# Performance work log

Measured on AMD Instinct MI355X. Metric: run time of the kernel, lower is better.

## Reference

```python
import jax, jax.numpy as jnp
import numpy as np

C = 2            # var_cardinality
ALPHA2 = 0.5     # global alpha2 skip coefficient referenced by the original module
A_FTOV = 0.5     # alpha_damping_FtoV
A_VTOF = 0.5     # alpha_damping_VtoF
SHIFT = 1e-19    # shifted ReLU offset (avoids log(0) in exp-space MLP)

V = 1_000_000    # num variables
F = 2_000_000    # num factors (pairwise)
E = 2 * F        # num factor->var edges


def setup_inputs() -> dict:
    key = jax.random.key(0)
    ks = jax.random.split(key, 6)
    # pairwise factors: factor f owns edges 2f (its dim-0 var) and 2f+1 (its dim-1 var)
    fac_idx = jnp.repeat(jnp.arange(F, dtype=jnp.int32), 2)          # [E]
    var_idx = jax.random.randint(ks[0], (E,), 0, V, dtype=jnp.int32)  # [E]
    edge_var_dim = jnp.tile(jnp.array([0, 1], dtype=jnp.int32), F)    # [E]
    eye = jnp.eye(C, dtype=jnp.float32)
    zc = jnp.zeros((C,), dtype=jnp.float32)
    return dict(
        prv_varToFactor_messages=jax.random.normal(ks[1], (E, C), dtype=jnp.float32),
        prv_factorToVar_messages=jax.random.normal(ks[2], (E, C), dtype=jnp.float32),
        prv_factor_beliefs=jax.random.normal(ks[3], (F, C, C), dtype=jnp.float32),
        factor_potentials=jax.random.normal(ks[4], (F, C, C), dtype=jnp.float32),
        W5=eye, b5=zc, W6=eye, b6=zc,          # mlp3 (factor->var), exact-BP init
        W7=eye, b7=zc, W8=eye, b8=zc,          # mlp4 (var->factor), exact-BP init
        alpha_mlp3=jnp.float32(ALPHA2), alpha_mlp4=jnp.float32(ALPHA2),
        fac_idx=fac_idx, var_idx=var_idx, edge_var_dim=edge_var_dim,
    )


def _mlp_exp_space(logm, W1, b1, W2, b2):
    # lne_mlp=True: exponentiate, run linear-relu-linear-shifted_relu, back to log space
    m = jnp.exp(logm)
    h = jax.nn.relu(m @ W1.T + b1)
    o = jax.nn.relu(h @ W2.T + b2) + SHIFT
    return jnp.log(o)


def _expand(msg, dim):
    # [E,C] per-edge message over its variable -> [E,C,C] over the factor's joint state,
    # broadcast along the factor dimension the edge does NOT own
    e0 = jnp.broadcast_to(msg[:, :, None], (msg.shape[0], C, C))
    e1 = jnp.broadcast_to(msg[:, None, :], (msg.shape[0], C, C))
    return jnp.where((dim == 0)[:, None, None], e0, e1)


def reference(prv_varToFactor_messages, prv_factorToVar_messages,
              prv_factor_beliefs, factor_potentials,
              W5, b5, W6, b6, W7, b7, W8, b8,
              alpha_mlp3, alpha_mlp4,
              fac_idx, var_idx, edge_var_dim):
    lse = jax.scipy.special.logsumexp
    # ---- factor -> variable messages (no double counting) ----
    mapped_fb = prv_factor_beliefs[fac_idx]                                  # gather [E,C,C]
    tmp = mapped_fb - _expand(prv_varToFactor_messages, edge_var_dim)        # subtract prv msg in log space
    marg = jnp.where((edge_var_dim == 0)[:, None],
                     lse(tmp, axis=2), lse(tmp, axis=1))                     # marginalize other var [E,C]
    ftv = alpha_mlp3 * marg + (1.0 - alpha_mlp3) * _mlp_exp_space(marg, W5, b5, W6, b6)
    ftv = A_FTOV * ftv + (1.0 - A_FTOV) * prv_factorToVar_messages           # damping
    ftv = ftv - lse(ftv, axis=1, keepdims=True)                              # normalize
    # ---- variable beliefs: log-space sum of incoming messages ----
    var_beliefs = jax.ops.segment_sum(ftv, var_idx, num_segments=V)          # [V,C]
    # ---- variable -> factor messages (no double counting) ----
    mapped_vb = var_beliefs[var_idx]                                         # gather [E,C]
    vtf_exact = mapped_vb - ftv
    vtf = alpha_mlp4 * vtf_exact + (1.0 - alpha_mlp4) * _mlp_exp_space(vtf_exact, W7, b7, W8, b8)
    vtf = A_VTOF * vtf + (1.0 - A_VTOF) * prv_varToFactor_messages           # damping
    vtf = vtf - lse(vtf, axis=1, keepdims=True)                              # normalize
    # ---- factor beliefs: scatter expanded messages + factor potentials ----
    expanded = _expand(vtf, edge_var_dim)                                    # [E,C,C]
    factor_beliefs = jax.ops.segment_sum(expanded, fac_idx, num_segments=F) + factor_potentials
    return vtf, ftv, var_beliefs, factor_beliefs
```

## Files before the change

### kernel.cpp

```cpp
#include <hip/hip_runtime.h>
#include <hip/hip_fp16.h>


typedef float vf4 __attribute__((ext_vector_type(4)));
typedef float vf2 __attribute__((ext_vector_type(2)));
typedef int   vi2 __attribute__((ext_vector_type(2)));

#define NB_SHIFT 13
#define VPB (1 << NB_SHIFT)
#define MAXNB 128
#define CAP 28
#define FACT_PER_BLK 1024
#define BIN_THREADS 256

__device__ __forceinline__ vf4 ntload4(const float* p) {
    return __builtin_nontemporal_load((const vf4*)p);
}
__device__ __forceinline__ vi2 ntload2i(const int* p) {
    return __builtin_nontemporal_load((const vi2*)p);
}
__device__ __forceinline__ void ntstore4(float* p, vf4 v) {
    __builtin_nontemporal_store(v, (vf4*)p);
}

__device__ __forceinline__ float lse2(float a, float b) {
    float mx = fmaxf(a, b);
    return mx + __logf(__expf(a - mx) + __expf(b - mx));
}

struct Mlp2 {
    float w00, w01, w10, w11, b0, b1;
    float u00, u01, u10, u11, c0, c1;
    __device__ __forceinline__ void load(const float* __restrict__ W1, const float* __restrict__ B1,
                                         const float* __restrict__ W2, const float* __restrict__ B2) {
        w00 = W1[0]; w01 = W1[1]; w10 = W1[2]; w11 = W1[3];
        b0 = B1[0]; b1 = B1[1];
        u00 = W2[0]; u01 = W2[1]; u10 = W2[2]; u11 = W2[3];
        c0 = B2[0]; c1 = B2[1];
    }
    __device__ __forceinline__ void apply(float& x0, float& x1) const {
        float m0 = __expf(x0), m1 = __expf(x1);
        float h0 = fmaxf(fmaf(w00, m0, fmaf(w01, m1, b0)), 0.f);
        float h1 = fmaxf(fmaf(w10, m0, fmaf(w11, m1, b1)), 0.f);
        float o0 = fmaxf(fmaf(u00, h0, fmaf(u01, h1, c0)), 0.f) + 1e-19f;
        float o1 = fmaxf(fmaf(u10, h0, fmaf(u11, h1, c1)), 0.f) + 1e-19f;
        x0 = __logf(o0);
        x1 = __logf(o1);
    }
};

__global__ void __launch_bounds__(BIN_THREADS) fg_pass1_bin(
    const float* __restrict__ fb,
    const float* __restrict__ pvtf,
    const float* __restrict__ pftv,
    const int* __restrict__ vidx,
    const float* __restrict__ W5, const float* __restrict__ b5,
    const float* __restrict__ W6, const float* __restrict__ b6,
    const float* __restrict__ alpha3p,
    float* __restrict__ out_ftv,
    float* __restrict__ out_vb,
    unsigned long long* __restrict__ bins,
    unsigned* __restrict__ cnt_t,
    int F, int NB, int NBLK)
{
    __shared__ unsigned long long stage[MAXNB * CAP];
    __shared__ unsigned cnt[MAXNB];

    const int tid = threadIdx.x;
    for (int i = tid; i < MAXNB; i += BIN_THREADS) cnt[i] = 0;
    __syncthreads();

    const float a3 = *alpha3p;
    Mlp2 mlp; mlp.load(W5, b5, W6, b6);

    const size_t base_f = (size_t)blockIdx.x * FACT_PER_BLK;

    for (int k = 0; k < FACT_PER_BLK; k += BIN_THREADS) {
        size_t f = base_f + k + tid;
        if (f < (size_t)F) {
            vf4 b  = ntload4(fb + 4 * f);
            vf4 pm = ntload4(pvtf + 4 * f);
            vf4 pf = ntload4(pftv + 4 * f);

            float m00 = lse2(b.x - pm.x, b.y - pm.x);
            float m01 = lse2(b.z - pm.y, b.w - pm.y);
            float m10 = lse2(b.x - pm.z, b.z - pm.z);
            float m11 = lse2(b.y - pm.w, b.w - pm.w);

            float n00 = m00, n01 = m01; mlp.apply(n00, n01);
            float n10 = m10, n11 = m11; mlp.apply(n10, n11);

            float t00 = 0.5f * fmaf(a3, m00, (1.f - a3) * n00) + 0.5f * pf.x;
            float t01 = 0.5f * fmaf(a3, m01, (1.f - a3) * n01) + 0.5f * pf.y;
            float t10 = 0.5f * fmaf(a3, m10, (1.f - a3) * n10) + 0.5f * pf.z;
            float t11 = 0.5f * fmaf(a3, m11, (1.f - a3) * n11) + 0.5f * pf.w;
            float l0 = lse2(t00, t01); t00 -= l0; t01 -= l0;
            float l1 = lse2(t10, t11); t10 -= l1; t11 -= l1;

            vf4 ot; ot.x = t00; ot.y = t01; ot.z = t10; ot.w = t11;
            *(vf4*)(out_ftv + 4 * f) = ot;

            vi2 vv = ntload2i(vidx + 2 * f);

            {
                int v = vv.x;
                int bk = v >> NB_SHIFT;
                unsigned pos = atomicAdd(&cnt[bk], 1u);
                if (pos < CAP) {
                    __half2 h = __floats2half2_rn(t00, t01);
                    unsigned hu = __builtin_bit_cast(unsigned, h);
                    unsigned loc = (unsigned)(v & (VPB - 1));
                    stage[bk * CAP + pos] = ((unsigned long long)loc << 32) | hu;
                } else {
                    atomicAdd(out_vb + 2 * (size_t)v,     t00);
                    atomicAdd(out_vb + 2 * (size_t)v + 1, t01);
                }
            }
            {
                int v = vv.y;
                int bk = v >> NB_SHIFT;
                unsigned pos = atomicAdd(&cnt[bk], 1u);
                if (pos < CAP) {
                    __half2 h = __floats2half2_rn(t10, t11);
                    unsigned hu = __builtin_bit_cast(unsigned, h);
                    unsigned loc = (unsigned)(v & (VPB - 1));
                    stage[bk * CAP + pos] = ((unsigned long long)loc << 32) | hu;
                } else {
                    atomicAdd(out_vb + 2 * (size_t)v,     t10);
                    atomicAdd(out_vb + 2 * (size_t)v + 1, t11);
                }
            }
        }
    }

    __syncthreads();

    const int w = blockIdx.x;
    for (int s = tid; s < NB * CAP; s += BIN_THREADS) {
        int bk = s / CAP;
        int i  = s - bk * CAP;
        unsigned stored = min(cnt[bk], (unsigned)CAP);
        if (i < (int)stored)
            bins[((size_t)bk * NBLK + w) * CAP + i] = stage[bk * CAP + i];
        if (i == 0)
            cnt_t[(size_t)bk * NBLK + w] = stored;
    }
}

__global__ void __launch_bounds__(256) fg_reduce_bins(
    const unsigned long long* __restrict__ bins,
    const unsigned* __restrict__ cnt_t,
    float* __restrict__ out_vb,
    int V, int NBLK)
{
    __shared__ float acc[VPB * 2];
    const int tid = threadIdx.x;
    const int b = blockIdx.x;

    for (int i = tid; i < VPB * 2; i += 256) acc[i] = 0.f;
    __syncthreads();

    const unsigned long long* bbase = bins + (size_t)b * NBLK * CAP;
    const unsigned* cbase = cnt_t + (size_t)b * NBLK;

    for (int w = tid; w < NBLK; w += 256) {
        unsigned c = cbase[w];
        const unsigned long long* p = bbase + (size_t)w * CAP;
        for (unsigned i = 0; i < c; ++i) {
            unsigned long long r = p[i];
            unsigned loc = (unsigned)(r >> 32);
            __half2 h = __builtin_bit_cast(__half2, (unsigned)(r & 0xffffffffu));
            float2 cv = __half22float2(h);
            atomicAdd(&acc[2 * loc],     cv.x);
            atomicAdd(&acc[2 * loc + 1], cv.y);
        }
    }
    __syncthreads();

    const int vbase = b << NB_SHIFT;
    for (int i = tid; i < VPB; i += 256) {
        int v = vbase + i;
        if (v < V) {
            float2 cur = *(float2*)(out_vb + 2 * (size_t)v);
            cur.x += acc[2 * i];
            cur.y += acc[2 * i + 1];
            *(float2*)(out_vb + 2 * (size_t)v) = cur;
        }
    }
}

__global__ void __launch_bounds__(256) fg_pass1_direct(
    const float* __restrict__ fb,
    const float* __restrict__ pvtf,
    const float* __restrict__ pftv,
    const int* __restrict__ vidx,
    const float* __restrict__ W5, const float* __restrict__ b5,
    const float* __restrict__ W6, const float* __restrict__ b6,
    const float* __restrict__ alpha3p,
    float* __restrict__ out_ftv,
    float* __restrict__ out_vb,
    int F)
{
    size_t f = (size_t)blockIdx.x * blockDim.x + threadIdx.x;
    if (f >= (size_t)F) return;

    const float a3 = *alpha3p;
    Mlp2 mlp; mlp.load(W5, b5, W6, b6);

    vf4 b  = ntload4(fb + 4 * f);
    vf4 pm = ntload4(pvtf + 4 * f);
    vf4 pf = ntload4(pftv + 4 * f);

    float m00 = lse2(b.x - pm.x, b.y - pm.x);
    float m01 = lse2(b.z - pm.y, b.w - pm.y);
    float m10 = lse2(b.x - pm.z, b.z - pm.z);
    float m11 = lse2(b.y - pm.w, b.w - pm.w);

    float n00 = m00, n01 = m01; mlp.apply(n00, n01);
    float n10 = m10, n11 = m11; mlp.apply(n10, n11);

    float t00 = 0.5f * fmaf(a3, m00, (1.f - a3) * n00) + 0.5f * pf.x;
    float t01 = 0.5f * fmaf(a3, m01, (1.f - a3) * n01) + 0.5f * pf.y;
    float t10 = 0.5f * fmaf(a3, m10, (1.f - a3) * n10) + 0.5f * pf.z;
    float t11 = 0.5f * fmaf(a3, m11, (1.f - a3) * n11) + 0.5f * pf.w;
    float l0 = lse2(t00, t01); t00 -= l0; t01 -= l0;
    float l1 = lse2(t10, t11); t10 -= l1; t11 -= l1;

    vf4 ot; ot.x = t00; ot.y = t01; ot.z = t10; ot.w = t11;
    *(vf4*)(out_ftv + 4 * f) = ot;

    vi2 vv = ntload2i(vidx + 2 * f);
    atomicAdd(out_vb + 2 * (size_t)vv.x,     t00);
    atomicAdd(out_vb + 2 * (size_t)vv.x + 1, t01);
    atomicAdd(out_vb + 2 * (size_t)vv.y,     t10);
    atomicAdd(out_vb + 2 * (size_t)vv.y + 1, t11);
}

__global__ void __launch_bounds__(256) fg_pass2(
    const float* __restrict__ ftv,
    const float* __restrict__ vb,
    const float* __restrict__ pvtf,
    const float* __restrict__ pot,
    const int* __restrict__ vidx,
    const float* __restrict__ W7, const float* __restrict__ b7,
    const float* __restrict__ W8, const float* __restrict__ b8,
    const float* __restrict__ alpha4p,
    float* __restrict__ out_vtf,
    float* __restrict__ out_fb,
    int F)
{
    size_t f = (size_t)blockIdx.x * blockDim.x + threadIdx.x;
    if (f >= (size_t)F) return;

    const float a4 = *alpha4p;
    Mlp2 mlp; mlp.load(W7, b7, W8, b8);

    vf4 t = ntload4(ftv + 4 * f);
    vi2 vv = ntload2i(vidx + 2 * f);
    float2 vb0 = *(const float2*)(vb + 2 * (size_t)vv.x);
    float2 vb1 = *(const float2*)(vb + 2 * (size_t)vv.y);

    float e00 = vb0.x - t.x, e01 = vb0.y - t.y;
    float e10 = vb1.x - t.z, e11 = vb1.y - t.w;

    float n00 = e00, n01 = e01; mlp.apply(n00, n01);
    float n10 = e10, n11 = e11; mlp.apply(n10, n11);

    vf4 pm = ntload4(pvtf + 4 * f);
    float v00 = 0.5f * fmaf(a4, e00, (1.f - a4) * n00) + 0.5f * pm.x;
    float v01 = 0.5f * fmaf(a4, e01, (1.f - a4) * n01) + 0.5f * pm.y;
    float v10 = 0.5f * fmaf(a4, e10, (1.f - a4) * n10) + 0.5f * pm.z;
    float v11 = 0.5f * fmaf(a4, e11, (1.f - a4) * n11) + 0.5f * pm.w;
    float l0 = lse2(v00, v01); v00 -= l0; v01 -= l0;
    float l1 = lse2(v10, v11); v10 -= l1; v11 -= l1;

    vf4 ov; ov.x = v00; ov.y = v01; ov.z = v10; ov.w = v11;
    ntstore4(out_vtf + 4 * f, ov);

    vf4 p = ntload4(pot + 4 * f);
    vf4 ob;
    ob.x = v00 + v10 + p.x;
    ob.y = v00 + v11 + p.y;
    ob.z = v01 + v10 + p.z;
    ob.w = v01 + v11 + p.w;
    ntstore4(out_fb + 4 * f, ob);
}

extern "C" void kernel_launch(void* const* d_in, const int* in_sizes, int n_in,
                              void* d_out, int out_size, void* d_ws, size_t ws_size,
                              hipStream_t stream) {
    const float* prv_vtf = (const float*)d_in[0];
    const float* prv_ftv = (const float*)d_in[1];
    const float* fbel    = (const float*)d_in[2];
    const float* pot     = (const float*)d_in[3];
    const float* W5 = (const float*)d_in[4];
    const float* b5 = (const float*)d_in[5];
    const float* W6 = (const float*)d_in[6];
    const float* b6 = (const float*)d_in[7];
    const float* W7 = (const float*)d_in[8];
    const float* b7 = (const float*)d_in[9];
    const float* W8 = (const float*)d_in[10];
    const float* b8 = (const float*)d_in[11];
    const float* a3 = (const float*)d_in[12];
    const float* a4 = (const float*)d_in[13];
    const int* var_idx = (const int*)d_in[15];

    const int E = in_sizes[0] / 2;
    const int F = in_sizes[2] / 4;
    const int V = (out_size - 4 * E - 4 * F) / 2;

    float* out_vtf = (float*)d_out;
    float* out_ftv = out_vtf + (size_t)E * 2;
    float* out_vb  = out_ftv + (size_t)E * 2;
    float* out_fb  = out_vb + (size_t)V * 2;

    const int NBLK = (F + FACT_PER_BLK - 1) / FACT_PER_BLK;
    const int NB   = (V + VPB - 1) >> NB_SHIFT;

    const size_t bins_bytes = (size_t)NB * NBLK * CAP * sizeof(unsigned long long);
    const size_t cnt_bytes  = (size_t)NB * NBLK * sizeof(unsigned);
    const bool use_bins = (NB <= MAXNB) && (ws_size >= bins_bytes + cnt_bytes);

    unsigned long long* bins = (unsigned long long*)d_ws;
    unsigned* cnt_t = (unsigned*)((char*)d_ws + bins_bytes);

    dim3 block(256);
    dim3 gridF((F + 255) / 256);

    hipMemsetAsync(out_vb, 0, (size_t)V * 2 * sizeof(float), stream);

    if (use_bins) {
        fg_pass1_bin<<<dim3(NBLK), dim3(BIN_THREADS), 0, stream>>>(
            fbel, prv_vtf, prv_ftv, var_idx,
            W5, b5, W6, b6, a3,
            out_ftv, out_vb, bins, cnt_t, F, NB, NBLK);
        fg_reduce_bins<<<dim3(NB), block, 0, stream>>>(
            bins, cnt_t, out_vb, V, NBLK);
    } else {
        fg_pass1_direct<<<gridF, block, 0, stream>>>(
            fbel, prv_vtf, prv_ftv, var_idx,
            W5, b5, W6, b6, a3,
            out_ftv, out_vb, F);
    }

    fg_pass2<<<gridF, block, 0, stream>>>(
        out_ftv, out_vb, prv_vtf, pot, var_idx,
        W7, b7, W8, b8, a4,
        out_vtf, out_fb, F);
}
```

Measured before the change: 414.7 us.

## Split bin reduction across multiple blocks per bucket with partial-sum pass

Replaces the single-block-per-bucket bin reduction (only NB≈123 blocks) with RSPLIT=4 blocks per bucket, each accumulating a slice of producer blocks into shared memory and writing a partial array. The partials are staged in the not-yet-written factor-belief output buffer, and a second small kernel sums them into the variable beliefs. Work inside each block is also spread finer, with threads handling groups of four records instead of whole cells. This raises parallelism for a latency-bound reduction at the cost of an extra launch and an extra write and read of partials.

```diff
diff --git a/kernel.cpp b/kernel.cpp
--- a/kernel.cpp
+++ b/kernel.cpp
@@ -3,8 +3,8 @@
 
 
 typedef float vf4 __attribute__((ext_vector_type(4)));
-typedef float vf2 __attribute__((ext_vector_type(2)));
 typedef int   vi2 __attribute__((ext_vector_type(2)));
+typedef unsigned long long u64;
 
 #define NB_SHIFT 13
 #define VPB (1 << NB_SHIFT)
@@ -12,6 +12,7 @@
 #define CAP 28
 #define FACT_PER_BLK 1024
 #define BIN_THREADS 256
+#define RSPLIT 4
 
 __device__ __forceinline__ vf4 ntload4(const float* p) {
     return __builtin_nontemporal_load((const vf4*)p);
@@ -59,11 +60,11 @@
     const float* __restrict__ alpha3p,
     float* __restrict__ out_ftv,
     float* __restrict__ out_vb,
-    unsigned long long* __restrict__ bins,
+    u64* __restrict__ bins,
     unsigned* __restrict__ cnt_t,
     int F, int NB, int NBLK)
 {
-    __shared__ unsigned long long stage[MAXNB * CAP];
+    __shared__ u64 stage[MAXNB * CAP];
     __shared__ unsigned cnt[MAXNB];
 
     const int tid = threadIdx.x;
@@ -110,7 +111,7 @@
                     __half2 h = __floats2half2_rn(t00, t01);
                     unsigned hu = __builtin_bit_cast(unsigned, h);
                     unsigned loc = (unsigned)(v & (VPB - 1));
-                    stage[bk * CAP + pos] = ((unsigned long long)loc << 32) | hu;
+                    stage[bk * CAP + pos] = ((u64)loc << 32) | hu;
                 } else {
                     atomicAdd(out_vb + 2 * (size_t)v,     t00);
                     atomicAdd(out_vb + 2 * (size_t)v + 1, t01);
@@ -124,7 +125,7 @@
                     __half2 h = __floats2half2_rn(t10, t11);
                     unsigned hu = __builtin_bit_cast(unsigned, h);
                     unsigned loc = (unsigned)(v & (VPB - 1));
-                    stage[bk * CAP + pos] = ((unsigned long long)loc << 32) | hu;
+                    stage[bk * CAP + pos] = ((u64)loc << 32) | hu;
                 } else {
                     atomicAdd(out_vb + 2 * (size_t)v,     t10);
                     atomicAdd(out_vb + 2 * (size_t)v + 1, t11);
@@ -147,8 +148,85 @@
     }
 }
 
+__global__ void __launch_bounds__(256) fg_reduce_p1(
+    const u64* __restrict__ bins,
+    const unsigned* __restrict__ cnt_t,
+    float* __restrict__ partials,
+    int NBLK)
+{
+    __shared__ float acc[VPB * 2];
+    const int tid = threadIdx.x;
+    const int s = blockIdx.x, S = gridDim.x;
+    const int b = blockIdx.y;
+
+    for (int i = tid; i < VPB * 2; i += 256) acc[i] = 0.f;
+    __syncthreads();
+
+    const int w0 = (int)(((long long)NBLK * s) / S);
+    const int w1 = (int)(((long long)NBLK * (s + 1)) / S);
+    const int nw = w1 - w0;
+
+    const u64* bbase = bins + ((size_t)b * NBLK + w0) * CAP;
+    const unsigned* cbase = cnt_t + (size_t)b * NBLK + w0;
+
+    const int QUADS = CAP / 4;
+    for (int idx = tid; idx < nw * QUADS; idx += 256) {
+        int cell = idx / QUADS;
+        int q = idx - cell * QUADS;
+        unsigned c = cbase[cell];
+        int i0 = q * 4;
+        if ((unsigned)i0 >= c) continue;
+        const u64* p = bbase + (size_t)cell * CAP + i0;
+        u64 r0 = p[0], r1 = p[1], r2 = p[2], r3 = p[3];
+#define PROC(r, k)                                                        \
+        if ((unsigned)(i0 + (k)) < c) {                                   \
+            unsigned loc = (unsigned)((r) >> 32);                         \
+            __half2 h = __builtin_bit_cast(__half2,                       \
+                                           (unsigned)((r) & 0xffffffffu));\
+            float2 cv = __half22float2(h);                                \
+            atomicAdd(&acc[2 * loc],     cv.x);                           \
+            atomicAdd(&acc[2 * loc + 1], cv.y);                           \
+        }
+        PROC(r0, 0) PROC(r1, 1) PROC(r2, 2) PROC(r3, 3)
+#undef PROC
+    }
+    __syncthreads();
+
+    float* dst = partials + ((size_t)b * S + s) * (VPB * 2);
+    for (int i = tid * 4; i < VPB * 2; i += 256 * 4)
+        *(float4*)(dst + i) = *(const float4*)(acc + i);
+}
+
+__global__ void __launch_bounds__(256) fg_reduce_p2(
+    const float* __restrict__ partials,
+    float* __restrict__ out_vb,
+    int V, int S)
+{
+    const int b = blockIdx.y;
+    const int i = blockIdx.x * 1024 + threadIdx.x * 4;
+    const long long base_elem = (((long long)b) << (NB_SHIFT + 1)) + i;
+    if (base_elem >= (long long)V * 2) return;
+
+    const float* p = partials + ((size_t)b * S) * (VPB * 2) + i;
+    float4 sum = *(const float4*)p;
+    for (int s = 1; s < S; ++s) {
+        float4 t = *(const float4*)(p + (size_t)s * (VPB * 2));
+        sum.x += t.x; sum.y += t.y; sum.z += t.z; sum.w += t.w;
+    }
+    float* dst = out_vb + base_elem;
+    if (base_elem + 4 <= (long long)V * 2) {
+        float4 cur = *(const float4*)dst;
+        sum.x += cur.x; sum.y += cur.y; sum.z += cur.z; sum.w += cur.w;
+        *(float4*)dst = sum;
+    } else {
+        float* sp = (float*)&sum;
+        for (int k = 0; base_elem + k < (long long)V * 2 && k < 4; ++k)
+            dst[k] += sp[k];
+    }
+}
+
 __global__ void __launch_bounds__(256) fg_reduce_bins(
-    const unsigned long long* __restrict__ bins,
+    const u64* __restrict__ bins,
     const unsigned* __restrict__ cnt_t,
     float* __restrict__ out_vb,
     int V, int NBLK)
@@ -160,14 +238,14 @@
     for (int i = tid; i < VPB * 2; i += 256) acc[i] = 0.f;
     __syncthreads();
 
-    const unsigned long long* bbase = bins + (size_t)b * NBLK * CAP;
+    const u64* bbase = bins + (size_t)b * NBLK * CAP;
     const unsigned* cbase = cnt_t + (size_t)b * NBLK;
 
     for (int w = tid; w < NBLK; w += 256) {
         unsigned c = cbase[w];
-        const unsigned long long* p = bbase + (size_t)w * CAP;
+        const u64* p = bbase + (size_t)w * CAP;
         for (unsigned i = 0; i < c; ++i) {
-            unsigned long long r = p[i];
+            u64 r = p[i];
             unsigned loc = (unsigned)(r >> 32);
             __half2 h = __builtin_bit_cast(__half2, (unsigned)(r & 0xffffffffu));
             float2 cv = __half22float2(h);
@@ -317,11 +395,14 @@
     const int NBLK = (F + FACT_PER_BLK - 1) / FACT_PER_BLK;
     const int NB   = (V + VPB - 1) >> NB_SHIFT;
 
-    const size_t bins_bytes = (size_t)NB * NBLK * CAP * sizeof(unsigned long long);
+    const size_t bins_bytes = (size_t)NB * NBLK * CAP * sizeof(u64);
     const size_t cnt_bytes  = (size_t)NB * NBLK * sizeof(unsigned);
     const bool use_bins = (NB <= MAXNB) && (ws_size >= bins_bytes + cnt_bytes);
 
-    unsigned long long* bins = (unsigned long long*)d_ws;
+    const bool use_split = use_bins &&
+        ((size_t)NB * RSPLIT * (VPB * 2) <= (size_t)F * 4);
+
+    u64* bins = (u64*)d_ws;
     unsigned* cnt_t = (unsigned*)((char*)d_ws + bins_bytes);
 
     dim3 block(256);
@@ -334,8 +415,16 @@
             fbel, prv_vtf, prv_ftv, var_idx,
             W5, b5, W6, b6, a3,
             out_ftv, out_vb, bins, cnt_t, F, NB, NBLK);
-        fg_reduce_bins<<<dim3(NB), block, 0, stream>>>(
-            bins, cnt_t, out_vb, V, NBLK);
+        if (use_split) {
+            float* partials = out_fb;
+            fg_reduce_p1<<<dim3(RSPLIT, NB), block, 0, stream>>>(
+                bins, cnt_t, partials, NBLK);
+            fg_reduce_p2<<<dim3((VPB * 2) / 1024, NB), block, 0, stream>>>(
+                partials, out_vb, V, RSPLIT);
+        } else {
+            fg_reduce_bins<<<dim3(NB), block, 0, stream>>>(
+                bins, cnt_t, out_vb, V, NBLK);
+        }
     } else {
         fg_pass1_direct<<<gridF, block, 0, stream>>>(
             fbel, prv_vtf, prv_ftv, var_idx,
```

New measurement: 411.1 us. No clear change (-0.9%).
